# Kernel optimization log

Hardware: AMD Instinct MI355X
Metric: run time of the kernel (lower is better)

Reference implementation:

```python
import jax, jax.numpy as jnp
import numpy as np

DEPTH = 4
CHUNK = 16


def tp(a, b):
    """Graded tensor (outer) product on flattened levels: (...,m)x(...,n)->(...,m*n)."""
    return jnp.einsum('...i,...j->...ij', a, b).reshape(*a.shape[:-1], a.shape[-1] * b.shape[-1])


def ta_mul(a, b):
    """Truncated tensor-algebra product of two group-like elements (implicit level-0 == 1).
    a, b: lists of levels 1..D, level k flattened to C**k."""
    out = []
    for k in range(len(a)):
        t = a[k] + b[k]
        for i in range(k):
            t = t + tp(a[i], b[k - 1 - i])
        out.append(t)
    return out


def ta_mulz(a, b):
    """Product when both elements have level-0 == 0."""
    out = []
    for k in range(len(a)):
        t = jnp.zeros_like(a[k])
        for i in range(k):
            t = t + tp(a[i], b[k - 1 - i])
        out.append(t)
    return out


def ta_exp(a):
    """exp of a level-0-free element, truncated at DEPTH; returns levels 1..D (level-0 == 1 implicit)."""
    out = list(a)
    p = a
    fact = 1.0
    for m in range(2, len(a) + 1):
        p = ta_mulz(a, p)
        fact *= m
        out = [o + q / fact for o, q in zip(out, p)]
    return out


def ta_log(s):
    """Truncated log of group-like element g = 1 + s; input s = levels 1..D of g."""
    out = list(s)
    p = s
    sign = 1.0
    for m in range(2, len(s) + 1):
        p = ta_mulz(s, p)
        sign = -sign
        out = [o + (sign / m) * q for o, q in zip(out, p)]
    return out


def bch(a, b):
    """BCH merge: log(exp(a) (x) exp(b)) in the truncated algebra."""
    return ta_log(ta_mul(ta_exp(a), ta_exp(b)))


def exp_l1(d):
    """exp of a pure level-1 element d (shape (...,C)): level k = d^(x)k / k!."""
    levels = [d]
    cur = d
    fact = 1.0
    for k in range(2, DEPTH + 1):
        cur = tp(cur, d)
        fact *= k
        levels.append(cur / fact)
    return levels


def chunk_signatures(inc):
    """inc: (B, N, L, C) per-chunk increments -> signature levels [(B,N,C), (B,N,C^2), ...]
    via Chen: sig = exp(d_1) (x) ... (x) exp(d_L)."""
    carry0 = tuple(exp_l1(inc[:, :, 0]))
    xs = jnp.moveaxis(inc[:, :, 1:], 2, 0)  # (L-1, B, N, C)
    def step(carry, d):
        return tuple(ta_mul(list(carry), exp_l1(d))), None
    carry, _ = jax.lax.scan(step, carry0, xs)
    return list(carry)


def hillis_steele(levels):
    """Inclusive associative scan over chunk dim (axis=1) with BCH merge.
    bch(0, b) == b exactly, so zero-padding handles the boundary."""
    N = levels[0].shape[1]
    pref = levels
    d = 1
    while d < N:
        shifted = [jnp.concatenate([jnp.zeros_like(l[:, :d]), l[:, :-d]], axis=1) for l in pref]
        pref = bch(shifted, pref)
        d *= 2
    return pref


def _forward(x, W1, b1, W2, b2):
    B, T, Cin = x.shape
    t = jnp.linspace(0.0, 1.0, T, dtype=x.dtype)
    path = jnp.concatenate([x, jnp.broadcast_to(t[None, :, None], (B, T, 1)).astype(x.dtype)], axis=-1)
    C = Cin + 1
    # basepoint=True: path starts at 0, so increments are diff of [0; path]
    inc = jnp.diff(path, axis=1, prepend=jnp.zeros((B, 1, C), x.dtype))
    N = T // CHUNK
    inc = inc.reshape(B, N, CHUNK, C)
    sig = chunk_signatures(inc)          # levels 1..D, (B,N,C^k)
    logl = ta_log(sig)                   # truncated log-signature per chunk
    pref = hillis_steele(logl)           # inclusive BCH prefix scan
    flat = jnp.concatenate(pref, axis=-1)  # (B, N, mem_dim)
    pooled = flat.mean(axis=1)           # readout_pool == 'mean'
    h = jnp.maximum(pooled @ W1 + b1, 0.0)
    return h @ W2 + b2


def setup_inputs() -> dict:
    key = jax.random.key(0)
    k0, k1, k2 = jax.random.split(key, 3)
    B, T, Cin = 8, 2048, 7
    mem_dim, H, out_dim = 4680, 256, 1
    x = jax.random.normal(k0, (B, T, Cin), dtype=jnp.float32)
    W1 = jax.random.normal(k1, (mem_dim, H), dtype=jnp.float32) * (1.0 / np.sqrt(mem_dim))
    b1 = jnp.zeros((H,), jnp.float32)
    W2 = jax.random.normal(k2, (H, out_dim), dtype=jnp.float32) * (1.0 / np.sqrt(H))
    b2 = jnp.zeros((out_dim,), jnp.float32)
    return {"x": x, "W1": W1, "b1": b1, "W2": W2, "b2": b2}


def reference(x, W1, b1, W2, b2):
    return _forward(x, W1, b1, W2, b2)
```

## Files before the change

kernel.cpp:

```cpp
#include <hip/hip_runtime.h>


#define MEM   4680
#define NG    32
#define TLEN  2048

#define P3OFF 72
#define P4OFF 648
#define SIGSZ 5256

__device__ __forceinline__ void load_inc(const float* __restrict__ x, int b, int g,
                                         float* sInc, int tid) {
    for (int e = tid; e < 512; e += 256) {
        int s = e >> 3, c = e & 7;
        int t = g * 64 + s;
        float v;
        if (c < 7) {
            float cur  = x[(b * TLEN + t) * 7 + c];
            float prev = (t > 0) ? x[(b * TLEN + t - 1) * 7 + c] : 0.f;
            v = cur - prev;
        } else v = (t > 0) ? (1.f / 2047.f) : 0.f;
        sInc[e] = v;
    }
}

__device__ __forceinline__ void chunk_step(const float* dch, float* sA, float* U, int tid) {
    float* loc3 = U;
    float* loc2 = U + 576;
    float* loc1 = U + 640;
    const int i1 = tid >> 6, j1 = (tid >> 3) & 7, k1 = tid & 7;
    const int row1 = tid >> 3, row2 = row1 + 32;
    const int jk = tid & 63;
    const int pos2 = tid + 256, i2 = pos2 >> 6;
    float p1a = 0.f, l2a = 0.f, l3a = 0.f, p1b = 0.f, l2b = 0.f, l3b = 0.f;
    float Sa[8], Sb[8];
#pragma unroll
    for (int l = 0; l < 8; l++) { Sa[l] = 0.f; Sb[l] = 0.f; }
#pragma unroll
    for (int t = 0; t < 16; t++) {
        const float* dr = dch + t * 8;
        float di1 = dr[i1], di2 = dr[i2], dj = dr[j1], dk = dr[k1];
        float ga = l3a + dk * (l2a * 0.5f + dj * (p1a * (1.f/6.f) + di1 * (1.f/24.f)));
        float gb = l3b + dk * (l2b * 0.5f + dj * (p1b * (1.f/6.f) + di2 * (1.f/24.f)));
#pragma unroll
        for (int l = 0; l < 8; l++) { float dv = dr[l]; Sa[l] += ga * dv; Sb[l] += gb * dv; }
        l3a += dk * (l2a + dj * (p1a * 0.5f + di1 * (1.f/6.f)));
        l3b += dk * (l2b + dj * (p1b * 0.5f + di2 * (1.f/6.f)));
        l2a += (p1a + di1 * 0.5f) * dj;
        l2b += (p1b + di2 * 0.5f) * dj;
        p1a += di1; p1b += di2;
    }
    loc3[row1 * 9 + k1] = l3a;
    loc3[row2 * 9 + k1] = l3b;
    if (k1 == 0) { loc2[row1] = l2a; loc2[row2] = l2b; }
    if (jk == 0) { loc1[i1] = p1a; loc1[i2] = p1b; }
    __syncthreads();
    float a1 = sA[i1], a2 = sA[8 + row1], a3 = sA[P3OFF + row1 * 9 + k1];
    float c1_ = sA[i2], c2_ = sA[8 + row2], c3_ = sA[P3OFF + row2 * 9 + k1];
    const float* l3p = &loc3[jk * 9];
    const float* l2p = &loc2[k1 * 8];
    float n4a[8], n4b[8];
#pragma unroll
    for (int l = 0; l < 8; l++) {
        float v3 = l3p[l], v2 = l2p[l], v1 = loc1[l];
        n4a[l] = sA[P4OFF + tid * 9 + l]  + Sa[l] + a1 * v3 + a2 * v2 + a3 * v1;
        n4b[l] = sA[P4OFF + pos2 * 9 + l] + Sb[l] + c1_ * v3 + c2_ * v2 + c3_ * v1;
    }
    float n3a = a3 + l3a + a1 * loc2[jk] + a2 * loc1[k1];
    float n3b = c3_ + l3b + c1_ * loc2[jk] + c2_ * loc1[k1];
    float n2v = 0.f, n1v = 0.f;
    if (tid < 64) n2v = sA[8 + tid] + loc2[tid] + sA[tid >> 3] * loc1[tid & 7];
    if (tid < 8)  n1v = sA[tid] + loc1[tid];
    __syncthreads();
#pragma unroll
    for (int l = 0; l < 8; l++) { sA[P4OFF + tid * 9 + l] = n4a[l]; sA[P4OFF + pos2 * 9 + l] = n4b[l]; }
    sA[P3OFF + row1 * 9 + k1] = n3a;
    sA[P3OFF + row2 * 9 + k1] = n3b;
    if (tid < 64) sA[8 + tid] = n2v;
    if (tid < 8)  sA[tid] = n1v;
    __syncthreads();
}

__global__ __launch_bounds__(256) void sig_totals_kernel(const float* __restrict__ x,
                                                         float* __restrict__ T) {
    int blk = blockIdx.x;
    int b = blk >> 5, g = blk & 31;
    int tid = threadIdx.x;

    __shared__ __attribute__((aligned(16))) float sInc[512];
    __shared__ __attribute__((aligned(16))) float sA[SIGSZ];
    __shared__ __attribute__((aligned(16))) float U[648];

    load_inc(x, b, g, sInc, tid);
    for (int m = tid; m < SIGSZ; m += 256) sA[m] = 0.f;
    __syncthreads();
    for (int c = 0; c < 4; c++) chunk_step(&sInc[c * 128], sA, U, tid);

    size_t base = (size_t)blk * MEM;
    for (int m = tid; m < MEM; m += 256) {
        float v;
        if (m < 72) v = sA[m];
        else if (m < 584) { int e = m - 72;  v = sA[P3OFF + (e >> 3) * 9 + (e & 7)]; }
        else              { int e = m - 584; v = sA[P4OFF + (e >> 3) * 9 + (e & 7)]; }
        T[base + m] = v;
    }
}

__global__ __launch_bounds__(256) void scan_fused_kernel(const float* __restrict__ T,
                                                         float* __restrict__ P) {
    int bx = blockIdx.x;
    int b = bx >> 4, s = bx & 15;
    int tid = threadIdx.x;

    __shared__ float st1[NG][8];
    __shared__ float st2[NG][64];
    __shared__ float st3[NG][32];
    __shared__ float sp1[NG][8];
    __shared__ float sp2[NG][64];
    __shared__ float sp3[NG][32];

    int bBase = b * NG;
    {
        int g = tid >> 3, i = tid & 7;
        st1[g][i] = T[(size_t)(bBase + g) * MEM + i];
    }
    for (int m = tid; m < NG * 64; m += 256) {
        int g = m >> 6, e = m & 63;
        st2[g][e] = T[(size_t)(bBase + g) * MEM + 8 + e];
    }
    for (int m = tid; m < NG * 32; m += 256) {
        int g = m >> 5, e = m & 31;
        st3[g][e] = T[(size_t)(bBase + g) * MEM + 72 + s * 32 + e];
    }
    __syncthreads();

    if (tid < 64) {
        int i = tid >> 3, k = tid & 7;
        float p1acc = 0.f, p2acc = 0.f;
        for (int g = 0; g < NG; g++) {
            sp2[g][tid] = p2acc;
            if (k == 0) sp1[g][i] = p1acc;
            if (s == 0) {
                size_t prow = (size_t)(bBase + g) * MEM;
                P[prow + 8 + tid] = p2acc;
                if (k == 0) P[prow + i] = p1acc;
            }
            p2acc += st2[g][tid] + p1acc * st1[g][k];
            p1acc += st1[g][i];
        }
    }
    __syncthreads();
    if (tid < 32) {
        int ijk = s * 32 + tid;
        int i = ijk >> 6, jk = ijk & 63, ij = ijk >> 3, k = ijk & 7;
        float acc3 = 0.f;
        for (int g = 0; g < NG; g++) {
            sp3[g][tid] = acc3;
            P[(size_t)(bBase + g) * MEM + 72 + ijk] = acc3;
            acc3 += st3[g][tid] + sp1[g][i] * st2[g][jk] + sp2[g][ij] * st1[g][k];
        }
    }
    __syncthreads();
    {
        int m = s * 256 + tid;
        int i = m >> 9, jkl = m & 511, ij = m >> 6, kl = m & 63, l = m & 7;
        int p3loc = tid >> 3;
        float acc4 = 0.f;
#pragma unroll 4
        for (int g = 0; g < NG; g++) {
            size_t row = (size_t)(bBase + g) * MEM;
            P[row + 584 + m] = acc4;
            acc4 += T[row + 584 + m]
                  + sp1[g][i] * T[row + 72 + jkl]
                  + sp2[g][ij] * st2[g][kl]
                  + sp3[g][p3loc] * st1[g][l];
        }
    }
}

__global__ __launch_bounds__(256) void apply_log_pool_kernel(const float* __restrict__ x,
                                                             const float* __restrict__ P,
                                                             float* __restrict__ partial) {
    int blk = blockIdx.x;
    int b = blk >> 5, g = blk & 31;
    int tid = threadIdx.x;

    __shared__ __attribute__((aligned(16))) float sInc[512];
    __shared__ __attribute__((aligned(16))) float sA[SIGSZ];
    __shared__ __attribute__((aligned(16))) float sP[SIGSZ];
    __shared__ __attribute__((aligned(16))) float U[648];
    __shared__ __attribute__((aligned(16))) float sR[648];
    __shared__ __attribute__((aligned(16))) float sQ23[576];

    load_inc(x, b, g, sInc, tid);
    {
        size_t base = (size_t)blk * MEM;
        if (tid < 72) sP[tid] = P[base + tid];
        for (int e = tid; e < 512; e += 256)
            sP[P3OFF + (e >> 3) * 9 + (e & 7)] = P[base + 72 + e];
        for (int e = tid; e < 4096; e += 256)
            sP[P4OFF + (e >> 3) * 9 + (e & 7)] = P[base + 584 + e];
    }
    for (int m = tid; m < SIGSZ; m += 256) sA[m] = 0.f;
    __syncthreads();

    const int i1 = tid >> 6, j1 = (tid >> 3) & 7, k1 = tid & 7;
    const int row1 = tid >> 3, row2 = row1 + 32;
    const int jk = tid & 63;
    const int pos2 = tid + 256, i2 = pos2 >> 6;

    float pool4a[8], pool4b[8];
#pragma unroll
    for (int l = 0; l < 8; l++) { pool4a[l] = 0.f; pool4b[l] = 0.f; }
    float pool3a = 0.f, pool3b = 0.f, pool2 = 0.f, pool1 = 0.f;

    for (int c = 0; c < 4; c++) {
        chunk_step(&sInc[c * 128], sA, U, tid);

        float a1 = sP[i1], a2 = sP[8 + row1], a3 = sP[P3OFF + row1 * 9 + k1];
        float c1_ = sP[i2], c2_ = sP[8 + row2], c3_ = sP[P3OFF + row2 * 9 + k1];
        const float* q3p = &sA[P3OFF + jk * 9];
        const float* q2p = &sA[8 + k1 * 8];
        float R4a[8], R4b[8];
#pragma unroll
        for (int l = 0; l < 8; l++) {
            float v3 = q3p[l], v2 = q2p[l], v1 = sA[l];
            R4a[l] = sP[P4OFF + tid * 9 + l]  + sA[P4OFF + tid * 9 + l]  + a1 * v3 + a2 * v2 + a3 * v1;
            R4b[l] = sP[P4OFF + pos2 * 9 + l] + sA[P4OFF + pos2 * 9 + l] + c1_ * v3 + c2_ * v2 + c3_ * v1;
        }
        float R3a = a3 + sA[P3OFF + row1 * 9 + k1] + a1 * sA[8 + jk] + a2 * sA[k1];
        float R3b = c3_ + sA[P3OFF + row2 * 9 + k1] + c1_ * sA[8 + jk] + c2_ * sA[k1];
        float R2v = 0.f, R1v = 0.f;
        if (tid < 64) R2v = sP[8 + tid] + sA[8 + tid] + sP[tid >> 3] * sA[tid & 7];
        if (tid < 8)  R1v = sP[tid] + sA[tid];

        sR[P3OFF + row1 * 9 + k1] = R3a;
        sR[P3OFF + row2 * 9 + k1] = R3b;
        if (tid < 64) sR[8 + tid] = R2v;
        if (tid < 8)  sR[tid] = R1v;
        __syncthreads();

        float q23a = sR[i1] * sR[8 + jk] + sR[8 + row1] * sR[k1];
        float q23b = sR[i2] * sR[8 + jk] + sR[8 + row2] * sR[k1];
        sQ23[row1 * 9 + k1] = q23a;
        sQ23[row2 * 9 + k1] = q23b;
        __syncthreads();

        {
            float s1ia = sR[i1], s1ib = sR[i2], s1j = sR[j1], s1k = sR[k1];
            float s2ija = sR[8 + row1], s2ijb = sR[8 + row2];
            const float* r3p = &sR[P3OFF + jk * 9];
            const float* r2p = &sR[8 + k1 * 8];
            const float* q23p = &sQ23[jk * 9];
#pragma unroll
            for (int l = 0; l < 8; l++) {
                float s1l = sR[l];
                float p22 = s1k * s1l;
                float p24a = s1ia * r3p[l] + s2ija * r2p[l] + R3a * s1l;
                float p24b = s1ib * r3p[l] + s2ijb * r2p[l] + R3b * s1l;
                float p34a = s1ia * q23p[l] + s2ija * p22;
                float p34b = s1ib * q23p[l] + s2ijb * p22;
                float p44a = s1ia * s1j * p22;
                float p44b = s1ib * s1j * p22;
                pool4a[l] += R4a[l] - 0.5f * p24a + (1.f/3.f) * p34a - 0.25f * p44a;
                pool4b[l] += R4b[l] - 0.5f * p24b + (1.f/3.f) * p34b - 0.25f * p44b;
            }
            pool3a += R3a - 0.5f * q23a + (1.f/3.f) * s1ia * s1j * s1k;
            pool3b += R3b - 0.5f * q23b + (1.f/3.f) * s1ib * s1j * s1k;
            if (tid < 64) pool2 += R2v - 0.5f * sR[tid >> 3] * sR[tid & 7];
            if (tid < 8)  pool1 += R1v;
        }
        __syncthreads();
    }

    {
        float* pb = partial + (size_t)blk * MEM;
        float4 va0 = make_float4(pool4a[0], pool4a[1], pool4a[2], pool4a[3]);
        float4 va1 = make_float4(pool4a[4], pool4a[5], pool4a[6], pool4a[7]);
        float4 vb0 = make_float4(pool4b[0], pool4b[1], pool4b[2], pool4b[3]);
        float4 vb1 = make_float4(pool4b[4], pool4b[5], pool4b[6], pool4b[7]);
        float4* d1 = (float4*)(pb + 584 + tid * 8);
        d1[0] = va0; d1[1] = va1;
        float4* d2 = (float4*)(pb + 584 + (tid + 256) * 8);
        d2[0] = vb0; d2[1] = vb1;
        pb[72 + tid] = pool3a;
        pb[72 + tid + 256] = pool3b;
        if (tid < 64) pb[8 + tid] = pool2;
        if (tid < 8)  pb[tid] = pool1;
    }
}

__global__ __launch_bounds__(256) void gemv1_kernel(const float* __restrict__ partial,
                                                    const float* __restrict__ W1,
                                                    float* __restrict__ hpart) {
    int kc = blockIdx.x;
    int tid = threadIdx.x;
    int k0 = kc * 32;
    __shared__ float sp[8][32];
    {
        int b = tid >> 5, k = tid & 31;
        float sum = 0.f;
        if (k0 + k < MEM) {
            for (int g = 0; g < NG; g++)
                sum += partial[(size_t)(b * NG + g) * MEM + k0 + k];
        }
        sp[b][k] = sum * (1.f / 128.f);
    }
    __syncthreads();
    float acc[8];
#pragma unroll
    for (int b = 0; b < 8; b++) acc[b] = 0.f;
    int kend = (k0 + 32 < MEM) ? 32 : (MEM - k0);
    for (int k = 0; k < kend; k++) {
        float wv = W1[(size_t)(k0 + k) * 256 + tid];
#pragma unroll
        for (int b = 0; b < 8; b++) acc[b] += sp[b][k] * wv;
    }
#pragma unroll
    for (int b = 0; b < 8; b++) hpart[(size_t)kc * 2048 + b * 256 + tid] = acc[b];
}

__global__ __launch_bounds__(256) void final_kernel(const float* __restrict__ hpart,
                                                    const float* __restrict__ b1,
                                                    const float* __restrict__ W2,
                                                    const float* __restrict__ b2,
                                                    float* __restrict__ outp) {
    int b = blockIdx.x;
    int tid = threadIdx.x;
    float v = 0.f;
    for (int kc = 0; kc < 147; kc++) v += hpart[(size_t)kc * 2048 + b * 256 + tid];
    v += b1[tid];
    v = fmaxf(v, 0.f) * W2[tid];
    __shared__ float sRed[256];
    sRed[tid] = v;
    __syncthreads();
    for (int s = 128; s > 0; s >>= 1) {
        if (tid < s) sRed[tid] += sRed[tid + s];
        __syncthreads();
    }
    if (tid == 0) outp[b] = sRed[0] + b2[0];
}

extern "C" void kernel_launch(void* const* d_in, const int* in_sizes, int n_in,
                              void* d_out, int out_size, void* d_ws, size_t ws_size,
                              hipStream_t stream) {
    const float* x  = (const float*)d_in[0];
    const float* W1 = (const float*)d_in[1];
    const float* b1 = (const float*)d_in[2];
    const float* W2 = (const float*)d_in[3];
    const float* b2 = (const float*)d_in[4];
    float* out = (float*)d_out;

    float* ws = (float*)d_ws;
    float* T       = ws;
    float* P       = T + (size_t)256 * MEM;
    float* partial = P + (size_t)256 * MEM;
    float* hpart   = partial + (size_t)256 * MEM;

    sig_totals_kernel<<<256, 256, 0, stream>>>(x, T);
    scan_fused_kernel<<<128, 256, 0, stream>>>(T, P);
    apply_log_pool_kernel<<<256, 256, 0, stream>>>(x, P, partial);
    gemv1_kernel<<<147, 256, 0, stream>>>(partial, W1, hpart);
    final_kernel<<<8, 256, 0, stream>>>(hpart, b1, W2, b2, out);
}
```

Before: 126.8 us.

## Split per-chunk signature and log work across 1024 blocks with group fold

```diff
diff --git a/kernel.cpp b/kernel.cpp
--- a/kernel.cpp
+++ b/kernel.cpp
@@ -4,33 +4,37 @@
 #define MEM   4680
 #define NG    32
 #define TLEN  2048
-
 #define P3OFF 72
 #define P4OFF 648
 #define SIGSZ 5256
 
-__device__ __forceinline__ void load_inc(const float* __restrict__ x, int b, int g,
-                                         float* sInc, int tid) {
-    for (int e = tid; e < 512; e += 256) {
-        int s = e >> 3, c = e & 7;
-        int t = g * 64 + s;
+__device__ __forceinline__ void load_padded(float* dst, const float* __restrict__ src, int tid) {
+    if (tid < 72) dst[tid] = src[tid];
+    for (int e = tid; e < 512; e += 256) dst[P3OFF + (e >> 3) * 9 + (e & 7)] = src[72 + e];
+    for (int e = tid; e < 4096; e += 256) dst[P4OFF + (e >> 3) * 9 + (e & 7)] = src[584 + e];
+}
+
+__global__ __launch_bounds__(256) void chunk_sig_kernel(const float* __restrict__ x,
+                                                        float* __restrict__ Q) {
+    int blk = blockIdx.x;
+    int b = blk >> 7, n = blk & 127;
+    int tid = threadIdx.x;
+    __shared__ float dch[128];
+    if (tid < 128) {
+        int s = tid >> 3, c = tid & 7;
+        int t = n * 16 + s;
         float v;
         if (c < 7) {
             float cur  = x[(b * TLEN + t) * 7 + c];
             float prev = (t > 0) ? x[(b * TLEN + t - 1) * 7 + c] : 0.f;
             v = cur - prev;
         } else v = (t > 0) ? (1.f / 2047.f) : 0.f;
-        sInc[e] = v;
-    }
-}
-
-__device__ __forceinline__ void chunk_step(const float* dch, float* sA, float* U, int tid) {
-    float* loc3 = U;
-    float* loc2 = U + 576;
-    float* loc1 = U + 640;
+        dch[tid] = v;
+    }
+    __syncthreads();
+
     const int i1 = tid >> 6, j1 = (tid >> 3) & 7, k1 = tid & 7;
     const int row1 = tid >> 3, row2 = row1 + 32;
-    const int jk = tid & 63;
     const int pos2 = tid + 256, i2 = pos2 >> 6;
     float p1a = 0.f, l2a = 0.f, l3a = 0.f, p1b = 0.f, l2b = 0.f, l3b = 0.f;
     float Sa[8], Sb[8];
@@ -38,7 +42,7 @@
     for (int l = 0; l < 8; l++) { Sa[l] = 0.f; Sb[l] = 0.f; }
 #pragma unroll
     for (int t = 0; t < 16; t++) {
-        const float* dr = dch + t * 8;
+        const float* dr = &dch[t * 8];
         float di1 = dr[i1], di2 = dr[i2], dj = dr[j1], dk = dr[k1];
         float ga = l3a + dk * (l2a * 0.5f + dj * (p1a * (1.f/6.f) + di1 * (1.f/24.f)));
         float gb = l3b + dk * (l2b * 0.5f + dj * (p1b * (1.f/6.f) + di2 * (1.f/24.f)));
@@ -50,63 +54,70 @@
         l2b += (p1b + di2 * 0.5f) * dj;
         p1a += di1; p1b += di2;
     }
-    loc3[row1 * 9 + k1] = l3a;
-    loc3[row2 * 9 + k1] = l3b;
-    if (k1 == 0) { loc2[row1] = l2a; loc2[row2] = l2b; }
-    if (jk == 0) { loc1[i1] = p1a; loc1[i2] = p1b; }
-    __syncthreads();
-    float a1 = sA[i1], a2 = sA[8 + row1], a3 = sA[P3OFF + row1 * 9 + k1];
-    float c1_ = sA[i2], c2_ = sA[8 + row2], c3_ = sA[P3OFF + row2 * 9 + k1];
-    const float* l3p = &loc3[jk * 9];
-    const float* l2p = &loc2[k1 * 8];
-    float n4a[8], n4b[8];
-#pragma unroll
-    for (int l = 0; l < 8; l++) {
-        float v3 = l3p[l], v2 = l2p[l], v1 = loc1[l];
-        n4a[l] = sA[P4OFF + tid * 9 + l]  + Sa[l] + a1 * v3 + a2 * v2 + a3 * v1;
-        n4b[l] = sA[P4OFF + pos2 * 9 + l] + Sb[l] + c1_ * v3 + c2_ * v2 + c3_ * v1;
-    }
-    float n3a = a3 + l3a + a1 * loc2[jk] + a2 * loc1[k1];
-    float n3b = c3_ + l3b + c1_ * loc2[jk] + c2_ * loc1[k1];
-    float n2v = 0.f, n1v = 0.f;
-    if (tid < 64) n2v = sA[8 + tid] + loc2[tid] + sA[tid >> 3] * loc1[tid & 7];
-    if (tid < 8)  n1v = sA[tid] + loc1[tid];
-    __syncthreads();
-#pragma unroll
-    for (int l = 0; l < 8; l++) { sA[P4OFF + tid * 9 + l] = n4a[l]; sA[P4OFF + pos2 * 9 + l] = n4b[l]; }
-    sA[P3OFF + row1 * 9 + k1] = n3a;
-    sA[P3OFF + row2 * 9 + k1] = n3b;
-    if (tid < 64) sA[8 + tid] = n2v;
-    if (tid < 8)  sA[tid] = n1v;
-    __syncthreads();
-}
-
-__global__ __launch_bounds__(256) void sig_totals_kernel(const float* __restrict__ x,
-                                                         float* __restrict__ T) {
+    size_t base = (size_t)blk * MEM;
+    float4* d1 = (float4*)(Q + base + 584 + tid * 8);
+    d1[0] = make_float4(Sa[0], Sa[1], Sa[2], Sa[3]);
+    d1[1] = make_float4(Sa[4], Sa[5], Sa[6], Sa[7]);
+    float4* d2 = (float4*)(Q + base + 584 + pos2 * 8);
+    d2[0] = make_float4(Sb[0], Sb[1], Sb[2], Sb[3]);
+    d2[1] = make_float4(Sb[4], Sb[5], Sb[6], Sb[7]);
+    Q[base + 72 + tid] = l3a;
+    Q[base + 72 + pos2] = l3b;
+    if (k1 == 0) { Q[base + 8 + row1] = l2a; Q[base + 8 + row2] = l2b; }
+    if ((tid & 63) == 0) { Q[base + i1] = p1a; Q[base + i2] = p1b; }
+}
+
+__global__ __launch_bounds__(256) void group_fold_kernel(float* __restrict__ Q) {
     int blk = blockIdx.x;
-    int b = blk >> 5, g = blk & 31;
-    int tid = threadIdx.x;
-
-    __shared__ __attribute__((aligned(16))) float sInc[512];
+    int tid = threadIdx.x;
     __shared__ __attribute__((aligned(16))) float sA[SIGSZ];
-    __shared__ __attribute__((aligned(16))) float U[648];
-
-    load_inc(x, b, g, sInc, tid);
-    for (int m = tid; m < SIGSZ; m += 256) sA[m] = 0.f;
-    __syncthreads();
-    for (int c = 0; c < 4; c++) chunk_step(&sInc[c * 128], sA, U, tid);
-
-    size_t base = (size_t)blk * MEM;
-    for (int m = tid; m < MEM; m += 256) {
-        float v;
-        if (m < 72) v = sA[m];
-        else if (m < 584) { int e = m - 72;  v = sA[P3OFF + (e >> 3) * 9 + (e & 7)]; }
-        else              { int e = m - 584; v = sA[P4OFF + (e >> 3) * 9 + (e & 7)]; }
-        T[base + m] = v;
-    }
-}
-
-__global__ __launch_bounds__(256) void scan_fused_kernel(const float* __restrict__ T,
+    __shared__ __attribute__((aligned(16))) float sB[SIGSZ];
+
+    const int i1 = tid >> 6, k1 = tid & 7;
+    const int row1 = tid >> 3, row2 = row1 + 32;
+    const int jk = tid & 63;
+    const int pos2 = tid + 256, i2 = pos2 >> 6;
+
+    size_t base0 = (size_t)blk * 4 * MEM;
+    load_padded(sA, Q + base0, tid);
+
+    for (int c = 1; c < 4; c++) {
+        load_padded(sB, Q + base0 + (size_t)c * MEM, tid);
+        __syncthreads();
+        float a1 = sA[i1], a2 = sA[8 + row1], a3 = sA[P3OFF + row1 * 9 + k1];
+        float c1_ = sA[i2], c2_ = sA[8 + row2], c3_ = sA[P3OFF + row2 * 9 + k1];
+        const float* b3p = &sB[P3OFF + jk * 9];
+        const float* b2p = &sB[8 + k1 * 8];
+        float n4a[8], n4b[8];
+#pragma unroll
+        for (int l = 0; l < 8; l++) {
+            float v3 = b3p[l], v2 = b2p[l], v1 = sB[l];
+            n4a[l] = sA[P4OFF + tid * 9 + l]  + sB[P4OFF + tid * 9 + l]  + a1 * v3 + a2 * v2 + a3 * v1;
+            n4b[l] = sA[P4OFF + pos2 * 9 + l] + sB[P4OFF + pos2 * 9 + l] + c1_ * v3 + c2_ * v2 + c3_ * v1;
+        }
+        float n3a = a3 + sB[P3OFF + row1 * 9 + k1] + a1 * sB[8 + jk] + a2 * sB[k1];
+        float n3b = c3_ + sB[P3OFF + row2 * 9 + k1] + c1_ * sB[8 + jk] + c2_ * sB[k1];
+        float n2v = 0.f, n1v = 0.f;
+        if (tid < 64) n2v = sA[8 + tid] + sB[8 + tid] + sA[tid >> 3] * sB[tid & 7];
+        if (tid < 8)  n1v = sA[tid] + sB[tid];
+        __syncthreads();
+        size_t bc = base0 + (size_t)c * MEM;
+#pragma unroll
+        for (int l = 0; l < 8; l++) { sA[P4OFF + tid * 9 + l] = n4a[l]; sA[P4OFF + pos2 * 9 + l] = n4b[l]; }
+        float4* d1 = (float4*)(Q + bc + 584 + tid * 8);
+        d1[0] = make_float4(n4a[0], n4a[1], n4a[2], n4a[3]);
+        d1[1] = make_float4(n4a[4], n4a[5], n4a[6], n4a[7]);
+        float4* d2 = (float4*)(Q + bc + 584 + pos2 * 8);
+        d2[0] = make_float4(n4b[0], n4b[1], n4b[2], n4b[3]);
+        d2[1] = make_float4(n4b[4], n4b[5], n4b[6], n4b[7]);
+        sA[P3OFF + row1 * 9 + k1] = n3a; Q[bc + 72 + tid] = n3a;
+        sA[P3OFF + row2 * 9 + k1] = n3b; Q[bc + 72 + pos2] = n3b;
+        if (tid < 64) { sA[8 + tid] = n2v; Q[bc + 8 + tid] = n2v; }
+        if (tid < 8)  { sA[tid] = n1v;    Q[bc + tid] = n1v; }
+    }
+}
+
+__global__ __launch_bounds__(256) void scan_fused_kernel(const float* __restrict__ Q,
                                                          float* __restrict__ P) {
     int bx = blockIdx.x;
     int b = bx >> 4, s = bx & 15;
@@ -120,17 +131,18 @@
     __shared__ float sp3[NG][32];
 
     int bBase = b * NG;
+    size_t qb = (size_t)b * 128;
     {
         int g = tid >> 3, i = tid & 7;
-        st1[g][i] = T[(size_t)(bBase + g) * MEM + i];
+        st1[g][i] = Q[(qb + g * 4 + 3) * MEM + i];
     }
     for (int m = tid; m < NG * 64; m += 256) {
         int g = m >> 6, e = m & 63;
-        st2[g][e] = T[(size_t)(bBase + g) * MEM + 8 + e];
+        st2[g][e] = Q[(qb + g * 4 + 3) * MEM + 8 + e];
     }
     for (int m = tid; m < NG * 32; m += 256) {
         int g = m >> 5, e = m & 31;
-        st3[g][e] = T[(size_t)(bBase + g) * MEM + 72 + s * 32 + e];
+        st3[g][e] = Q[(qb + g * 4 + 3) * MEM + 72 + s * 32 + e];
     }
     __syncthreads();
 
@@ -168,40 +180,29 @@
         float acc4 = 0.f;
 #pragma unroll 4
         for (int g = 0; g < NG; g++) {
-            size_t row = (size_t)(bBase + g) * MEM;
-            P[row + 584 + m] = acc4;
-            acc4 += T[row + 584 + m]
-                  + sp1[g][i] * T[row + 72 + jkl]
+            size_t trow = (qb + g * 4 + 3) * MEM;
+            P[(size_t)(bBase + g) * MEM + 584 + m] = acc4;
+            acc4 += Q[trow + 584 + m]
+                  + sp1[g][i] * Q[trow + 72 + jkl]
                   + sp2[g][ij] * st2[g][kl]
                   + sp3[g][p3loc] * st1[g][l];
         }
     }
 }
 
-__global__ __launch_bounds__(256) void apply_log_pool_kernel(const float* __restrict__ x,
-                                                             const float* __restrict__ P,
-                                                             float* __restrict__ partial) {
+__global__ __launch_bounds__(256) void apply_log_kernel(const float* __restrict__ Q,
+                                                        const float* __restrict__ P,
+                                                        float* __restrict__ part) {
     int blk = blockIdx.x;
-    int b = blk >> 5, g = blk & 31;
-    int tid = threadIdx.x;
-
-    __shared__ __attribute__((aligned(16))) float sInc[512];
-    __shared__ __attribute__((aligned(16))) float sA[SIGSZ];
+    int b = blk >> 7, n = blk & 127, g = n >> 2;
+    int tid = threadIdx.x;
     __shared__ __attribute__((aligned(16))) float sP[SIGSZ];
-    __shared__ __attribute__((aligned(16))) float U[648];
+    __shared__ __attribute__((aligned(16))) float sB[SIGSZ];
     __shared__ __attribute__((aligned(16))) float sR[648];
     __shared__ __attribute__((aligned(16))) float sQ23[576];
 
-    load_inc(x, b, g, sInc, tid);
-    {
-        size_t base = (size_t)blk * MEM;
-        if (tid < 72) sP[tid] = P[base + tid];
-        for (int e = tid; e < 512; e += 256)
-            sP[P3OFF + (e >> 3) * 9 + (e & 7)] = P[base + 72 + e];
-        for (int e = tid; e < 4096; e += 256)
-            sP[P4OFF + (e >> 3) * 9 + (e & 7)] = P[base + 584 + e];
-    }
-    for (int m = tid; m < SIGSZ; m += 256) sA[m] = 0.f;
+    load_padded(sP, P + (size_t)(b * NG + g) * MEM, tid);
+    load_padded(sB, Q + (size_t)blk * MEM, tid);
     __syncthreads();
 
     const int i1 = tid >> 6, j1 = (tid >> 3) & 7, k1 = tid & 7;
@@ -209,88 +210,83 @@
     const int jk = tid & 63;
     const int pos2 = tid + 256, i2 = pos2 >> 6;
 
-    float pool4a[8], pool4b[8];
-#pragma unroll
-    for (int l = 0; l < 8; l++) { pool4a[l] = 0.f; pool4b[l] = 0.f; }
-    float pool3a = 0.f, pool3b = 0.f, pool2 = 0.f, pool1 = 0.f;
-
-    for (int c = 0; c < 4; c++) {
-        chunk_step(&sInc[c * 128], sA, U, tid);
-
-        float a1 = sP[i1], a2 = sP[8 + row1], a3 = sP[P3OFF + row1 * 9 + k1];
-        float c1_ = sP[i2], c2_ = sP[8 + row2], c3_ = sP[P3OFF + row2 * 9 + k1];
-        const float* q3p = &sA[P3OFF + jk * 9];
-        const float* q2p = &sA[8 + k1 * 8];
-        float R4a[8], R4b[8];
+    float a1 = sP[i1], a2 = sP[8 + row1], a3 = sP[P3OFF + row1 * 9 + k1];
+    float c1_ = sP[i2], c2_ = sP[8 + row2], c3_ = sP[P3OFF + row2 * 9 + k1];
+    const float* b3p = &sB[P3OFF + jk * 9];
+    const float* b2p = &sB[8 + k1 * 8];
+    float R4a[8], R4b[8];
+#pragma unroll
+    for (int l = 0; l < 8; l++) {
+        float v3 = b3p[l], v2 = b2p[l], v1 = sB[l];
+        R4a[l] = sP[P4OFF + tid * 9 + l]  + sB[P4OFF + tid * 9 + l]  + a1 * v3 + a2 * v2 + a3 * v1;
+        R4b[l] = sP[P4OFF + pos2 * 9 + l] + sB[P4OFF + pos2 * 9 + l] + c1_ * v3 + c2_ * v2 + c3_ * v1;
+    }
+    float R3a = a3 + sB[P3OFF + row1 * 9 + k1] + a1 * sB[8 + jk] + a2 * sB[k1];
+    float R3b = c3_ + sB[P3OFF + row2 * 9 + k1] + c1_ * sB[8 + jk] + c2_ * sB[k1];
+    float R2v = 0.f, R1v = 0.f;
+    if (tid < 64) R2v = sP[8 + tid] + sB[8 + tid] + sP[tid >> 3] * sB[tid & 7];
+    if (tid < 8)  R1v = sP[tid] + sB[tid];
+
+    sR[P3OFF + row1 * 9 + k1] = R3a;
+    sR[P3OFF + row2 * 9 + k1] = R3b;
+    if (tid < 64) sR[8 + tid] = R2v;
+    if (tid < 8)  sR[tid] = R1v;
+    __syncthreads();
+
+    float q23a = sR[i1] * sR[8 + jk] + sR[8 + row1] * sR[k1];
+    float q23b = sR[i2] * sR[8 + jk] + sR[8 + row2] * sR[k1];
+    sQ23[row1 * 9 + k1] = q23a;
+    sQ23[row2 * 9 + k1] = q23b;
+    __syncthreads();
+
+    size_t base = (size_t)blk * MEM;
+    {
+        float s1ia = sR[i1], s1ib = sR[i2], s1j = sR[j1], s1k = sR[k1];
+        float s2ija = sR[8 + row1], s2ijb = sR[8 + row2];
+        const float* r3p = &sR[P3OFF + jk * 9];
+        const float* r2p = &sR[8 + k1 * 8];
+        const float* q23p = &sQ23[jk * 9];
+        float out4a[8], out4b[8];
 #pragma unroll
         for (int l = 0; l < 8; l++) {
-            float v3 = q3p[l], v2 = q2p[l], v1 = sA[l];
-            R4a[l] = sP[P4OFF + tid * 9 + l]  + sA[P4OFF + tid * 9 + l]  + a1 * v3 + a2 * v2 + a3 * v1;
-            R4b[l] = sP[P4OFF + pos2 * 9 + l] + sA[P4OFF + pos2 * 9 + l] + c1_ * v3 + c2_ * v2 + c3_ * v1;
-        }
-        float R3a = a3 + sA[P3OFF + row1 * 9 + k1] + a1 * sA[8 + jk] + a2 * sA[k1];
-        float R3b = c3_ + sA[P3OFF + row2 * 9 + k1] + c1_ * sA[8 + jk] + c2_ * sA[k1];
-        float R2v = 0.f, R1v = 0.f;
-        if (tid < 64) R2v = sP[8 + tid] + sA[8 + tid] + sP[tid >> 3] * sA[tid & 7];
-        if (tid < 8)  R1v = sP[tid] + sA[tid];
-
-        sR[P3OFF + row1 * 9 + k1] = R3a;
-        sR[P3OFF + row2 * 9 + k1] = R3b;
-        if (tid < 64) sR[8 + tid] = R2v;
-        if (tid < 8)  sR[tid] = R1v;
-        __syncthreads();
-
-        float q23a = sR[i1] * sR[8 + jk] + sR[8 + row1] * sR[k1];
-        float q23b = sR[i2] * sR[8 + jk] + sR[8 + row2] * sR[k1];
-        sQ23[row1 * 9 + k1] = q23a;
-        sQ23[row2 * 9 + k1] = q23b;
-        __syncthreads();
-
-        {
-            float s1ia = sR[i1], s1ib = sR[i2], s1j = sR[j1], s1k = sR[k1];
-            float s2ija = sR[8 + row1], s2ijb = sR[8 + row2];
-            const float* r3p = &sR[P3OFF + jk * 9];
-            const float* r2p = &sR[8 + k1 * 8];
-            const float* q23p = &sQ23[jk * 9];
-#pragma unroll
-            for (int l = 0; l < 8; l++) {
-                float s1l = sR[l];
-                float p22 = s1k * s1l;
-                float p24a = s1ia * r3p[l] + s2ija * r2p[l] + R3a * s1l;
-                float p24b = s1ib * r3p[l] + s2ijb * r2p[l] + R3b * s1l;
-                float p34a = s1ia * q23p[l] + s2ija * p22;
-                float p34b = s1ib * q23p[l] + s2ijb * p22;
-                float p44a = s1ia * s1j * p22;
-                float p44b = s1ib * s1j * p22;
-                pool4a[l] += R4a[l] - 0.5f * p24a + (1.f/3.f) * p34a - 0.25f * p44a;
-                pool4b[l] += R4b[l] - 0.5f * p24b + (1.f/3.f) * p34b - 0.25f * p44b;
-            }
-            pool3a += R3a - 0.5f * q23a + (1.f/3.f) * s1ia * s1j * s1k;
-            pool3b += R3b - 0.5f * q23b + (1.f/3.f) * s1ib * s1j * s1k;
-            if (tid < 64) pool2 += R2v - 0.5f * sR[tid >> 3] * sR[tid & 7];
-            if (tid < 8)  pool1 += R1v;
-        }
-        __syncthreads();
-    }
-
-    {
-        float* pb = partial + (size_t)blk * MEM;
-        float4 va0 = make_float4(pool4a[0], pool4a[1], pool4a[2], pool4a[3]);
-        float4 va1 = make_float4(pool4a[4], pool4a[5], pool4a[6], pool4a[7]);
-        float4 vb0 = make_float4(pool4b[0], pool4b[1], pool4b[2], pool4b[3]);
-        float4 vb1 = make_float4(pool4b[4], pool4b[5], pool4b[6], pool4b[7]);
-        float4* d1 = (float4*)(pb + 584 + tid * 8);
-        d1[0] = va0; d1[1] = va1;
-        float4* d2 = (float4*)(pb + 584 + (tid + 256) * 8);
-        d2[0] = vb0; d2[1] = vb1;
-        pb[72 + tid] = pool3a;
-        pb[72 + tid + 256] = pool3b;
-        if (tid < 64) pb[8 + tid] = pool2;
-        if (tid < 8)  pb[tid] = pool1;
-    }
-}
-
-__global__ __launch_bounds__(256) void gemv1_kernel(const float* __restrict__ partial,
+            float s1l = sR[l];
+            float p22 = s1k * s1l;
+            float p24a = s1ia * r3p[l] + s2ija * r2p[l] + R3a * s1l;
+            float p24b = s1ib * r3p[l] + s2ijb * r2p[l] + R3b * s1l;
+            float p34a = s1ia * q23p[l] + s2ija * p22;
+            float p34b = s1ib * q23p[l] + s2ijb * p22;
+            float p44a = s1ia * s1j * p22;
+            float p44b = s1ib * s1j * p22;
+            out4a[l] = R4a[l] - 0.5f * p24a + (1.f/3.f) * p34a - 0.25f * p44a;
+            out4b[l] = R4b[l] - 0.5f * p24b + (1.f/3.f) * p34b - 0.25f * p44b;
+        }
+        float4* d1 = (float4*)(part + base + 584 + tid * 8);
+        d1[0] = make_float4(out4a[0], out4a[1], out4a[2], out4a[3]);
+        d1[1] = make_float4(out4a[4], out4a[5], out4a[6], out4a[7]);
+        float4* d2 = (float4*)(part + base + 584 + pos2 * 8);
+        d2[0] = make_float4(out4b[0], out4b[1], out4b[2], out4b[3]);
+        d2[1] = make_float4(out4b[4], out4b[5], out4b[6], out4b[7]);
+        part[base + 72 + tid]  = R3a - 0.5f * q23a + (1.f/3.f) * s1ia * s1j * s1k;
+        part[base + 72 + pos2] = R3b - 0.5f * q23b + (1.f/3.f) * s1ib * s1j * s1k;
+        if (tid < 64) part[base + 8 + tid] = R2v - 0.5f * sR[tid >> 3] * sR[tid & 7];
+        if (tid < 8)  part[base + tid] = R1v;
+    }
+}
+
+__global__ __launch_bounds__(256) void pool_reduce_kernel(const float* __restrict__ part,
+                                                          float* __restrict__ pooled) {
+    int bx = blockIdx.x;
+    int b = bx / 19, sl = bx % 19;
+    int idx = sl * 256 + threadIdx.x;
+    if (idx >= MEM) return;
+    float s = 0.f;
+    const float* p = part + (size_t)b * 128 * MEM + idx;
+#pragma unroll 4
+    for (int n = 0; n < 128; n++) s += p[(size_t)n * MEM];
+    pooled[b * MEM + idx] = s * (1.f / 128.f);
+}
+
+__global__ __launch_bounds__(256) void gemv1_kernel(const float* __restrict__ pooled,
                                                     const float* __restrict__ W1,
                                                     float* __restrict__ hpart) {
     int kc = blockIdx.x;
@@ -299,12 +295,7 @@
     __shared__ float sp[8][32];
     {
         int b = tid >> 5, k = tid & 31;
-        float sum = 0.f;
-        if (k0 + k < MEM) {
-            for (int g = 0; g < NG; g++)
-                sum += partial[(size_t)(b * NG + g) * MEM + k0 + k];
-        }
-        sp[b][k] = sum * (1.f / 128.f);
+        sp[b][k] = (k0 + k < MEM) ? pooled[b * MEM + k0 + k] : 0.f;
     }
     __syncthreads();
     float acc[8];
@@ -352,14 +343,17 @@
     float* out = (float*)d_out;
 
     float* ws = (float*)d_ws;
-    float* T       = ws;
-    float* P       = T + (size_t)256 * MEM;
-    float* partial = P + (size_t)256 * MEM;
-    float* hpart   = partial + (size_t)256 * MEM;
-
-    sig_totals_kernel<<<256, 256, 0, stream>>>(x, T);
-    scan_fused_kernel<<<128, 256, 0, stream>>>(T, P);
-    apply_log_pool_kernel<<<256, 256, 0, stream>>>(x, P, partial);
-    gemv1_kernel<<<147, 256, 0, stream>>>(partial, W1, hpart);
+    float* Q      = ws;
+    float* P      = Q + (size_t)1024 * MEM;
+    float* part   = P + (size_t)256 * MEM;
+    float* pooled = part + (size_t)1024 * MEM;
+    float* hpart  = pooled + 8 * MEM;
+
+    chunk_sig_kernel<<<1024, 256, 0, stream>>>(x, Q);
+    group_fold_kernel<<<256, 256, 0, stream>>>(Q);
+    scan_fused_kernel<<<128, 256, 0, stream>>>(Q, P);
+    apply_log_kernel<<<1024, 256, 0, stream>>>(Q, P, part);
+    pool_reduce_kernel<<<8 * 19, 256, 0, stream>>>(part, pooled);
+    gemv1_kernel<<<147, 256, 0, stream>>>(pooled, W1, hpart);
     final_kernel<<<8, 256, 0, stream>>>(hpart, b1, W2, b2, out);
 }
```

After: 149.9 us. 1.18x slower.

## Split chunk groups into halves to double block count across signature kernels

Applied to the files above, without the earlier changes.

```diff
diff --git a/kernel.cpp b/kernel.cpp
--- a/kernel.cpp
+++ b/kernel.cpp
@@ -2,26 +2,63 @@
 
 
 #define MEM   4680
-#define NG    32
+#define HG    64
 #define TLEN  2048
-
 #define P3OFF 72
 #define P4OFF 648
 #define SIGSZ 5256
 
-__device__ __forceinline__ void load_inc(const float* __restrict__ x, int b, int g,
-                                         float* sInc, int tid) {
-    for (int e = tid; e < 512; e += 256) {
-        int s = e >> 3, c = e & 7;
-        int t = g * 64 + s;
-        float v;
-        if (c < 7) {
-            float cur  = x[(b * TLEN + t) * 7 + c];
-            float prev = (t > 0) ? x[(b * TLEN + t - 1) * 7 + c] : 0.f;
-            v = cur - prev;
-        } else v = (t > 0) ? (1.f / 2047.f) : 0.f;
-        sInc[e] = v;
-    }
+__device__ __forceinline__ void load_padded(float* dst, const float* __restrict__ src, int tid) {
+    if (tid < 72) dst[tid] = src[tid];
+    for (int e = tid; e < 512; e += 256) dst[P3OFF + (e >> 3) * 9 + (e & 7)] = src[72 + e];
+    for (int e = tid; e < 4096; e += 256) dst[P4OFF + (e >> 3) * 9 + (e & 7)] = src[584 + e];
+}
+
+__device__ __forceinline__ void load_inc32(const float* __restrict__ x, int b, int h,
+                                           float* sInc, int tid) {
+    int s = tid >> 3, c = tid & 7;
+    int t = h * 32 + s;
+    float v;
+    if (c < 7) {
+        float cur  = x[(b * TLEN + t) * 7 + c];
+        float prev = (t > 0) ? x[(b * TLEN + t - 1) * 7 + c] : 0.f;
+        v = cur - prev;
+    } else v = (t > 0) ? (1.f / 2047.f) : 0.f;
+    sInc[tid] = v;
+}
+
+#define CHUNK_RECUR(dch)                                                            \
+    float p1a = 0.f, l2a = 0.f, l3a = 0.f, p1b = 0.f, l2b = 0.f, l3b = 0.f;         \
+    float Sa[8], Sb[8];                                                             \
+    _Pragma("unroll")                                                               \
+    for (int l = 0; l < 8; l++) { Sa[l] = 0.f; Sb[l] = 0.f; }                       \
+    _Pragma("unroll")                                                               \
+    for (int t = 0; t < 16; t++) {                                                  \
+        const float* dr = (dch) + t * 8;                                            \
+        float di1 = dr[i1], di2 = dr[i2], dj = dr[j1], dk = dr[k1];                 \
+        float ga = l3a + dk * (l2a * 0.5f + dj * (p1a * (1.f/6.f) + di1 * (1.f/24.f))); \
+        float gb = l3b + dk * (l2b * 0.5f + dj * (p1b * (1.f/6.f) + di2 * (1.f/24.f))); \
+        _Pragma("unroll")                                                           \
+        for (int l = 0; l < 8; l++) { float dv = dr[l]; Sa[l] += ga * dv; Sb[l] += gb * dv; } \
+        l3a += dk * (l2a + dj * (p1a * 0.5f + di1 * (1.f/6.f)));                    \
+        l3b += dk * (l2b + dj * (p1b * 0.5f + di2 * (1.f/6.f)));                    \
+        l2a += (p1a + di1 * 0.5f) * dj;                                             \
+        l2b += (p1b + di2 * 0.5f) * dj;                                             \
+        p1a += di1; p1b += di2;                                                     \
+    }
+
+__device__ __forceinline__ void chunk_step_first(const float* dch, float* sA, int tid) {
+    const int i1 = tid >> 6, j1 = (tid >> 3) & 7, k1 = tid & 7;
+    const int row1 = tid >> 3, row2 = row1 + 32;
+    const int pos2 = tid + 256, i2 = pos2 >> 6;
+    CHUNK_RECUR(dch)
+#pragma unroll
+    for (int l = 0; l < 8; l++) { sA[P4OFF + tid * 9 + l] = Sa[l]; sA[P4OFF + pos2 * 9 + l] = Sb[l]; }
+    sA[P3OFF + row1 * 9 + k1] = l3a;
+    sA[P3OFF + row2 * 9 + k1] = l3b;
+    if (k1 == 0) { sA[8 + row1] = l2a; sA[8 + row2] = l2b; }
+    if ((tid & 63) == 0) { sA[i1] = p1a; sA[i2] = p1b; }
+    __syncthreads();
 }
 
 __device__ __forceinline__ void chunk_step(const float* dch, float* sA, float* U, int tid) {
@@ -32,24 +69,7 @@
     const int row1 = tid >> 3, row2 = row1 + 32;
     const int jk = tid & 63;
     const int pos2 = tid + 256, i2 = pos2 >> 6;
-    float p1a = 0.f, l2a = 0.f, l3a = 0.f, p1b = 0.f, l2b = 0.f, l3b = 0.f;
-    float Sa[8], Sb[8];
-#pragma unroll
-    for (int l = 0; l < 8; l++) { Sa[l] = 0.f; Sb[l] = 0.f; }
-#pragma unroll
-    for (int t = 0; t < 16; t++) {
-        const float* dr = dch + t * 8;
-        float di1 = dr[i1], di2 = dr[i2], dj = dr[j1], dk = dr[k1];
-        float ga = l3a + dk * (l2a * 0.5f + dj * (p1a * (1.f/6.f) + di1 * (1.f/24.f)));
-        float gb = l3b + dk * (l2b * 0.5f + dj * (p1b * (1.f/6.f) + di2 * (1.f/24.f)));
-#pragma unroll
-        for (int l = 0; l < 8; l++) { float dv = dr[l]; Sa[l] += ga * dv; Sb[l] += gb * dv; }
-        l3a += dk * (l2a + dj * (p1a * 0.5f + di1 * (1.f/6.f)));
-        l3b += dk * (l2b + dj * (p1b * 0.5f + di2 * (1.f/6.f)));
-        l2a += (p1a + di1 * 0.5f) * dj;
-        l2b += (p1b + di2 * 0.5f) * dj;
-        p1a += di1; p1b += di2;
-    }
+    CHUNK_RECUR(dch)
     loc3[row1 * 9 + k1] = l3a;
     loc3[row2 * 9 + k1] = l3b;
     if (k1 == 0) { loc2[row1] = l2a; loc2[row2] = l2b; }
@@ -81,20 +101,19 @@
     __syncthreads();
 }
 
-__global__ __launch_bounds__(256) void sig_totals_kernel(const float* __restrict__ x,
-                                                         float* __restrict__ T) {
+__global__ __launch_bounds__(256) void sig_half_kernel(const float* __restrict__ x,
+                                                       float* __restrict__ T) {
     int blk = blockIdx.x;
-    int b = blk >> 5, g = blk & 31;
-    int tid = threadIdx.x;
-
-    __shared__ __attribute__((aligned(16))) float sInc[512];
+    int b = blk >> 6, h = blk & 63;
+    int tid = threadIdx.x;
+    __shared__ __attribute__((aligned(16))) float sInc[256];
     __shared__ __attribute__((aligned(16))) float sA[SIGSZ];
     __shared__ __attribute__((aligned(16))) float U[648];
 
-    load_inc(x, b, g, sInc, tid);
-    for (int m = tid; m < SIGSZ; m += 256) sA[m] = 0.f;
-    __syncthreads();
-    for (int c = 0; c < 4; c++) chunk_step(&sInc[c * 128], sA, U, tid);
+    load_inc32(x, b, h, sInc, tid);
+    __syncthreads();
+    chunk_step_first(&sInc[0], sA, tid);
+    chunk_step(&sInc[128], sA, U, tid);
 
     size_t base = (size_t)blk * MEM;
     for (int m = tid; m < MEM; m += 256) {
@@ -112,23 +131,23 @@
     int b = bx >> 4, s = bx & 15;
     int tid = threadIdx.x;
 
-    __shared__ float st1[NG][8];
-    __shared__ float st2[NG][64];
-    __shared__ float st3[NG][32];
-    __shared__ float sp1[NG][8];
-    __shared__ float sp2[NG][64];
-    __shared__ float sp3[NG][32];
-
-    int bBase = b * NG;
-    {
-        int g = tid >> 3, i = tid & 7;
+    __shared__ float st1[HG][8];
+    __shared__ float st2[HG][64];
+    __shared__ float st3[HG][32];
+    __shared__ float sp1[HG][8];
+    __shared__ float sp2[HG][64];
+    __shared__ float sp3[HG][32];
+
+    int bBase = b * HG;
+    for (int m = tid; m < HG * 8; m += 256) {
+        int g = m >> 3, i = m & 7;
         st1[g][i] = T[(size_t)(bBase + g) * MEM + i];
     }
-    for (int m = tid; m < NG * 64; m += 256) {
+    for (int m = tid; m < HG * 64; m += 256) {
         int g = m >> 6, e = m & 63;
         st2[g][e] = T[(size_t)(bBase + g) * MEM + 8 + e];
     }
-    for (int m = tid; m < NG * 32; m += 256) {
+    for (int m = tid; m < HG * 32; m += 256) {
         int g = m >> 5, e = m & 31;
         st3[g][e] = T[(size_t)(bBase + g) * MEM + 72 + s * 32 + e];
     }
@@ -137,7 +156,7 @@
     if (tid < 64) {
         int i = tid >> 3, k = tid & 7;
         float p1acc = 0.f, p2acc = 0.f;
-        for (int g = 0; g < NG; g++) {
+        for (int g = 0; g < HG; g++) {
             sp2[g][tid] = p2acc;
             if (k == 0) sp1[g][i] = p1acc;
             if (s == 0) {
@@ -154,7 +173,7 @@
         int ijk = s * 32 + tid;
         int i = ijk >> 6, jk = ijk & 63, ij = ijk >> 3, k = ijk & 7;
         float acc3 = 0.f;
-        for (int g = 0; g < NG; g++) {
+        for (int g = 0; g < HG; g++) {
             sp3[g][tid] = acc3;
             P[(size_t)(bBase + g) * MEM + 72 + ijk] = acc3;
             acc3 += st3[g][tid] + sp1[g][i] * st2[g][jk] + sp2[g][ij] * st1[g][k];
@@ -167,7 +186,7 @@
         int p3loc = tid >> 3;
         float acc4 = 0.f;
 #pragma unroll 4
-        for (int g = 0; g < NG; g++) {
+        for (int g = 0; g < HG; g++) {
             size_t row = (size_t)(bBase + g) * MEM;
             P[row + 584 + m] = acc4;
             acc4 += T[row + 584 + m]
@@ -178,30 +197,22 @@
     }
 }
 
-__global__ __launch_bounds__(256) void apply_log_pool_kernel(const float* __restrict__ x,
-                                                             const float* __restrict__ P,
-                                                             float* __restrict__ partial) {
+__global__ __launch_bounds__(256) void apply_log_kernel(const float* __restrict__ x,
+                                                        const float* __restrict__ P,
+                                                        float* __restrict__ partial) {
     int blk = blockIdx.x;
-    int b = blk >> 5, g = blk & 31;
-    int tid = threadIdx.x;
-
-    __shared__ __attribute__((aligned(16))) float sInc[512];
+    int b = blk >> 6, h = blk & 63;
+    int tid = threadIdx.x;
+
+    __shared__ __attribute__((aligned(16))) float sInc[256];
     __shared__ __attribute__((aligned(16))) float sA[SIGSZ];
     __shared__ __attribute__((aligned(16))) float sP[SIGSZ];
     __shared__ __attribute__((aligned(16))) float U[648];
     __shared__ __attribute__((aligned(16))) float sR[648];
     __shared__ __attribute__((aligned(16))) float sQ23[576];
 
-    load_inc(x, b, g, sInc, tid);
-    {
-        size_t base = (size_t)blk * MEM;
-        if (tid < 72) sP[tid] = P[base + tid];
-        for (int e = tid; e < 512; e += 256)
-            sP[P3OFF + (e >> 3) * 9 + (e & 7)] = P[base + 72 + e];
-        for (int e = tid; e < 4096; e += 256)
-            sP[P4OFF + (e >> 3) * 9 + (e & 7)] = P[base + 584 + e];
-    }
-    for (int m = tid; m < SIGSZ; m += 256) sA[m] = 0.f;
+    load_inc32(x, b, h, sInc, tid);
+    load_padded(sP, P + (size_t)blk * MEM, tid);
     __syncthreads();
 
     const int i1 = tid >> 6, j1 = (tid >> 3) & 7, k1 = tid & 7;
@@ -214,17 +225,18 @@
     for (int l = 0; l < 8; l++) { pool4a[l] = 0.f; pool4b[l] = 0.f; }
     float pool3a = 0.f, pool3b = 0.f, pool2 = 0.f, pool1 = 0.f;
 
-    for (int c = 0; c < 4; c++) {
-        chunk_step(&sInc[c * 128], sA, U, tid);
+    for (int c = 0; c < 2; c++) {
+        if (c == 0) chunk_step_first(&sInc[0], sA, tid);
+        else        chunk_step(&sInc[128], sA, U, tid);
 
         float a1 = sP[i1], a2 = sP[8 + row1], a3 = sP[P3OFF + row1 * 9 + k1];
         float c1_ = sP[i2], c2_ = sP[8 + row2], c3_ = sP[P3OFF + row2 * 9 + k1];
-        const float* q3p = &sA[P3OFF + jk * 9];
-        const float* q2p = &sA[8 + k1 * 8];
+        const float* b3p = &sA[P3OFF + jk * 9];
+        const float* b2p = &sA[8 + k1 * 8];
         float R4a[8], R4b[8];
 #pragma unroll
         for (int l = 0; l < 8; l++) {
-            float v3 = q3p[l], v2 = q2p[l], v1 = sA[l];
+            float v3 = b3p[l], v2 = b2p[l], v1 = sA[l];
             R4a[l] = sP[P4OFF + tid * 9 + l]  + sA[P4OFF + tid * 9 + l]  + a1 * v3 + a2 * v2 + a3 * v1;
             R4b[l] = sP[P4OFF + pos2 * 9 + l] + sA[P4OFF + pos2 * 9 + l] + c1_ * v3 + c2_ * v2 + c3_ * v1;
         }
@@ -275,16 +287,14 @@
 
     {
         float* pb = partial + (size_t)blk * MEM;
-        float4 va0 = make_float4(pool4a[0], pool4a[1], pool4a[2], pool4a[3]);
-        float4 va1 = make_float4(pool4a[4], pool4a[5], pool4a[6], pool4a[7]);
-        float4 vb0 = make_float4(pool4b[0], pool4b[1], pool4b[2], pool4b[3]);
-        float4 vb1 = make_float4(pool4b[4], pool4b[5], pool4b[6], pool4b[7]);
         float4* d1 = (float4*)(pb + 584 + tid * 8);
-        d1[0] = va0; d1[1] = va1;
-        float4* d2 = (float4*)(pb + 584 + (tid + 256) * 8);
-        d2[0] = vb0; d2[1] = vb1;
+        d1[0] = make_float4(pool4a[0], pool4a[1], pool4a[2], pool4a[3]);
+        d1[1] = make_float4(pool4a[4], pool4a[5], pool4a[6], pool4a[7]);
+        float4* d2 = (float4*)(pb + 584 + pos2 * 8);
+        d2[0] = make_float4(pool4b[0], pool4b[1], pool4b[2], pool4b[3]);
+        d2[1] = make_float4(pool4b[4], pool4b[5], pool4b[6], pool4b[7]);
         pb[72 + tid] = pool3a;
-        pb[72 + tid + 256] = pool3b;
+        pb[72 + pos2] = pool3b;
         if (tid < 64) pb[8 + tid] = pool2;
         if (tid < 8)  pb[tid] = pool1;
     }
@@ -301,8 +311,9 @@
         int b = tid >> 5, k = tid & 31;
         float sum = 0.f;
         if (k0 + k < MEM) {
-            for (int g = 0; g < NG; g++)
-                sum += partial[(size_t)(b * NG + g) * MEM + k0 + k];
+#pragma unroll 4
+            for (int g = 0; g < HG; g++)
+                sum += partial[(size_t)(b * HG + g) * MEM + k0 + k];
         }
         sp[b][k] = sum * (1.f / 128.f);
     }
@@ -353,13 +364,13 @@
 
     float* ws = (float*)d_ws;
     float* T       = ws;
-    float* P       = T + (size_t)256 * MEM;
-    float* partial = P + (size_t)256 * MEM;
-    float* hpart   = partial + (size_t)256 * MEM;
-
-    sig_totals_kernel<<<256, 256, 0, stream>>>(x, T);
+    float* P       = T + (size_t)512 * MEM;
+    float* partial = P + (size_t)512 * MEM;
+    float* hpart   = partial + (size_t)512 * MEM;
+
+    sig_half_kernel<<<512, 256, 0, stream>>>(x, T);
     scan_fused_kernel<<<128, 256, 0, stream>>>(T, P);
-    apply_log_pool_kernel<<<256, 256, 0, stream>>>(x, P, partial);
+    apply_log_kernel<<<512, 256, 0, stream>>>(x, P, partial);
     gemv1_kernel<<<147, 256, 0, stream>>>(partial, W1, hpart);
     final_kernel<<<8, 256, 0, stream>>>(hpart, b1, W2, b2, out);
 }
```

New measurement: 141.6 us. +11.7%, slower.
